# Performance work log

Measured on AMD Instinct MI355X. Metric: run time of the kernel, lower is better.

The kernel has to match this reference:

```python
import jax, jax.numpy as jnp
import numpy as np

D_MODEL, D_K, D_V, H = 64, 32, 32, 8
B, HH, WW = 2, 48, 48
NQ = HH * WW


def setup_inputs() -> dict:
    key = jax.random.key(0)
    ks = jax.random.split(key, 16)
    inp = {
        "queries": jax.random.normal(ks[0], (B, D_MODEL, HH, WW), jnp.float32),
        "keys": jax.random.normal(ks[1], (B, D_MODEL, HH, WW), jnp.float32),
        "values": jax.random.normal(ks[2], (B, D_MODEL, HH, WW), jnp.float32),
        "attention_weights": jax.random.uniform(ks[3], (B, H, NQ, NQ), jnp.float32),
        "attention_mask": jax.random.randint(ks[4], (B, H, NQ, NQ), 0, 2) > 0,
        # Linear params: torch init normal(std=0.001) weights, zero bias
        "Wq": 0.001 * jax.random.normal(ks[5], (H * D_K, D_MODEL), jnp.float32),
        "bq": jnp.zeros((H * D_K,), jnp.float32),
        "Wk": 0.001 * jax.random.normal(ks[6], (H * D_K, D_MODEL), jnp.float32),
        "bk": jnp.zeros((H * D_K,), jnp.float32),
        "Wv": 0.001 * jax.random.normal(ks[7], (H * D_V, D_MODEL), jnp.float32),
        "bv": jnp.zeros((H * D_V,), jnp.float32),
        "Wo": 0.001 * jax.random.normal(ks[8], (D_MODEL, H * D_V), jnp.float32),
        "bo": jnp.zeros((D_MODEL,), jnp.float32),
    }
    return inp


def reference(queries, keys, values, attention_weights, attention_mask,
              Wq, bq, Wk, bk, Wv, bv, Wo, bo):
    b, c, hh, ww = queries.shape
    nq = hh * ww
    # torch .view(b, -1, c) on contiguous (b,c,h,w) is a raw row-major reshape
    qf = queries.reshape(b, nq, c)
    kf = keys.reshape(b, nq, c)
    vf = values.reshape(b, nq, c)
    q = (qf @ Wq.T + bq).reshape(b, nq, H, D_K).transpose(0, 2, 1, 3)  # b h nq dk
    k = (kf @ Wk.T + bk).reshape(b, nq, H, D_K).transpose(0, 2, 1, 3)  # b h nk dk
    v = (vf @ Wv.T + bv).reshape(b, nq, H, D_V).transpose(0, 2, 1, 3)  # b h nk dv
    att = jnp.einsum('bhqd,bhkd->bhqk', q, k) / np.sqrt(D_K).astype(np.float32)
    att = att * attention_weights
    att = jnp.where(attention_mask, -jnp.inf, att)
    att = jax.nn.softmax(att, axis=-1)  # dropout is identity in eval mode
    out = jnp.einsum('bhqk,bhkd->bhqd', att, v)
    out = out.transpose(0, 2, 1, 3).reshape(b, nq, H * D_V)
    out = out @ Wo.T + bo  # (b, nq, d_model)
    return out.reshape(b, -1, hh, ww)  # (b, d_model, h, w)
```

## Files before the change

kernel.cpp:

```cpp
#include <hip/hip_runtime.h>


typedef __attribute__((ext_vector_type(8))) short bf16x8;
typedef __attribute__((ext_vector_type(4))) short bf16x4;
typedef __attribute__((ext_vector_type(4))) float f32x4;
typedef __attribute__((ext_vector_type(4))) unsigned int u32x4;

constexpr int B_  = 2;
constexpr int H_  = 8;
constexpr int NQ_ = 2304;
constexpr int DM_ = 64;
constexpr int DK_ = 32;
constexpr int NT_ = NQ_ / 32;
constexpr int CH_ = 3;
constexpr int TPC_ = NT_ / CH_;
constexpr int GT_ = B_ * H_ * (NQ_ / 16);
constexpr float SCALE_ = 0.17677669529663687f;

constexpr size_t OFF_Q    = 0;
constexpr size_t OFF_K    = 2359296;
constexpr size_t OFF_V    = 4718592;
constexpr size_t OFF_OMID = 7077888;
constexpr size_t OFF_FLAG = 11796480;
constexpr size_t OFF_OP   = 11796736;
constexpr size_t OFF_ML   = 25952512;

static __device__ __forceinline__ unsigned short f2bf(float f) {
    unsigned int u = __builtin_bit_cast(unsigned int, f);
    u += 0x7fffu + ((u >> 16) & 1u);
    return (unsigned short)(u >> 16);
}

__global__ void detect_mask_k(const unsigned int* __restrict__ m, int* __restrict__ flag) {
    int t = threadIdx.x;
    unsigned int v = 0;
    for (int k = 0; k < 16; ++k) v |= m[t * 16 + k];
    unsigned long long b = __ballot(v > 1u);
    if (t == 0) *flag = (b != 0ull) ? 1 : 0;
}

__global__ __launch_bounds__(256) void proj_qkv_k(
    const float* __restrict__ qin, const float* __restrict__ kin, const float* __restrict__ vin,
    const float* __restrict__ Wq, const float* __restrict__ bq,
    const float* __restrict__ Wk, const float* __restrict__ bk,
    const float* __restrict__ Wv, const float* __restrict__ bv,
    unsigned short* __restrict__ Qbf, unsigned short* __restrict__ Kbf,
    unsigned short* __restrict__ Vbf)
{
    const int sel = blockIdx.y;
    const float* in  = sel == 0 ? qin : (sel == 1 ? kin : vin);
    const float* W   = sel == 0 ? Wq  : (sel == 1 ? Wk  : Wv);
    const float* bia = sel == 0 ? bq  : (sel == 1 ? bk  : bv);

    const int rt = blockIdx.x;
    const int b  = rt / (NQ_ / 8);
    const int r0 = (rt % (NQ_ / 8)) * 8;

    __shared__ alignas(16) float ins[8][64];
    const int t = threadIdx.x;
    const float4* src = reinterpret_cast<const float4*>(in + ((size_t)b * NQ_ + r0) * DM_);
    if (t < 128) reinterpret_cast<float4*>(&ins[0][0])[t] = src[t];
    __syncthreads();

    float acc[8];
#pragma unroll
    for (int r = 0; r < 8; ++r) acc[r] = 0.f;
    const float* wrow = W + t * DM_;
    for (int m = 0; m < DM_; ++m) {
        float wv = wrow[m];
#pragma unroll
        for (int r = 0; r < 8; ++r) acc[r] += ins[r][m] * wv;
    }
    const float bb = bia[t];
    const int h = t >> 5, d = t & 31;
#pragma unroll
    for (int r = 0; r < 8; ++r) {
        float o = acc[r] + bb;
        if (sel == 0) o *= SCALE_;
        unsigned short bvv = f2bf(o);
        if (sel == 2) Vbf[(((size_t)b * H_ + h) * DK_ + d) * NQ_ + (r0 + r)] = bvv;
        else {
            unsigned short* out = (sel == 1) ? Kbf : Qbf;
            out[(((size_t)b * H_ + h) * NQ_ + (r0 + r)) * DK_ + d] = bvv;
        }
    }
}

struct KVSlot {
    bf16x8 ka0, ka1;
    bf16x4 v00, v01, v10, v11;
};

static __device__ __forceinline__ void issue_kv(KVSlot& s,
    const unsigned short* __restrict__ kbase, const unsigned short* __restrict__ vbase,
    int j0, int l15, int hi)
{
    s.ka0 = *reinterpret_cast<const bf16x8*>(kbase + (size_t)(j0 + l15) * DK_ + 8 * hi);
    s.ka1 = *reinterpret_cast<const bf16x8*>(kbase + (size_t)(j0 + 16 + l15) * DK_ + 8 * hi);
    s.v00 = *reinterpret_cast<const bf16x4*>(vbase + (size_t)l15 * NQ_ + j0 + 4 * hi);
    s.v01 = *reinterpret_cast<const bf16x4*>(vbase + (size_t)l15 * NQ_ + j0 + 16 + 4 * hi);
    s.v10 = *reinterpret_cast<const bf16x4*>(vbase + (size_t)(16 + l15) * NQ_ + j0 + 4 * hi);
    s.v11 = *reinterpret_cast<const bf16x4*>(vbase + (size_t)(16 + l15) * NQ_ + j0 + 16 + 4 * hi);
}

template<bool ISBYTE> struct MSpan;
template<> struct MSpan<true>  { unsigned int m[8]; };
template<> struct MSpan<false> { u32x4 m[8]; };

static __device__ __forceinline__ void loadW(f32x4 (&W)[8], const float* __restrict__ p) {
#pragma unroll
    for (int u = 0; u < 4; ++u) {
        W[2 * u]     = *reinterpret_cast<const f32x4*>(p + 32 * u);
        W[2 * u + 1] = *reinterpret_cast<const f32x4*>(p + 32 * u + 16);
    }
}

static __device__ __forceinline__ void loadM(MSpan<true>& M, const unsigned char* __restrict__ p) {
#pragma unroll
    for (int u = 0; u < 4; ++u) {
        M.m[2 * u]     = *reinterpret_cast<const unsigned int*>(p + 32 * u);
        M.m[2 * u + 1] = *reinterpret_cast<const unsigned int*>(p + 32 * u + 16);
    }
}
static __device__ __forceinline__ void loadM(MSpan<false>& M, const unsigned char* __restrict__ p) {
#pragma unroll
    for (int u = 0; u < 4; ++u) {
        M.m[2 * u]     = *reinterpret_cast<const u32x4*>(p + 128 * u);
        M.m[2 * u + 1] = *reinterpret_cast<const u32x4*>(p + 128 * u + 64);
    }
}

static __device__ __forceinline__ unsigned int mb32(unsigned int v) { return v; }
static __device__ __forceinline__ unsigned int mb32(u32x4 v) {
    return (v[0] & 1u) | ((v[1] & 1u) << 8) | ((v[2] & 1u) << 16) | ((v[3] & 1u) << 24);
}

template<typename MT>
static __device__ __forceinline__ void consume_tile(
    const KVSlot& s, f32x4 w0, f32x4 w1, MT m0r, MT m1r, bf16x8 qb,
    f32x4& oacc0, f32x4& oacc1, float& lrun)
{
    const f32x4 zero = {0.f, 0.f, 0.f, 0.f};
    f32x4 s0 = __builtin_amdgcn_mfma_f32_16x16x32_bf16(s.ka0, qb, zero, 0, 0, 0);
    f32x4 s1 = __builtin_amdgcn_mfma_f32_16x16x32_bf16(s.ka1, qb, zero, 0, 0, 0);

    const unsigned int ba = mb32(m0r), bb = mb32(m1r);

    float p0[4], p1[4];
#pragma unroll
    for (int r = 0; r < 4; ++r) {
        float e0 = __expf(s0[r] * w0[r]);
        float e1 = __expf(s1[r] * w1[r]);
        p0[r] = ((ba >> (8 * r)) & 0xffu) ? 0.f : e0;
        p1[r] = ((bb >> (8 * r)) & 0xffu) ? 0.f : e1;
    }
    lrun += ((p0[0] + p0[1]) + (p0[2] + p0[3])) + ((p1[0] + p1[1]) + (p1[2] + p1[3]));

    bf16x8 pa;
#pragma unroll
    for (int r = 0; r < 4; ++r) {
        pa[r]     = (short)f2bf(p0[r]);
        pa[4 + r] = (short)f2bf(p1[r]);
    }
    bf16x8 vb0 = __builtin_shufflevector(s.v00, s.v01, 0, 1, 2, 3, 4, 5, 6, 7);
    bf16x8 vb1 = __builtin_shufflevector(s.v10, s.v11, 0, 1, 2, 3, 4, 5, 6, 7);
    oacc0 = __builtin_amdgcn_mfma_f32_16x16x32_bf16(pa, vb0, oacc0, 0, 0, 0);
    oacc1 = __builtin_amdgcn_mfma_f32_16x16x32_bf16(pa, vb1, oacc1, 0, 0, 0);
}

template<bool ISBYTE>
static __device__ __forceinline__ void consume4(
    KVSlot& sA, KVSlot& sB, const f32x4 (&W)[8], const MSpan<ISBYTE>& M,
    int tb, int t1,
    const unsigned short* __restrict__ kbase, const unsigned short* __restrict__ vbase,
    int l15, int hi, bf16x8 qb, f32x4& o0, f32x4& o1, float& lr)
{
    consume_tile(sA, W[0], W[1], M.m[0], M.m[1], qb, o0, o1, lr);
    if (tb + 2 < t1) issue_kv(sA, kbase, vbase, (tb + 2) * 32, l15, hi);
    consume_tile(sB, W[2], W[3], M.m[2], M.m[3], qb, o0, o1, lr);
    if (tb + 3 < t1) issue_kv(sB, kbase, vbase, (tb + 3) * 32, l15, hi);
    consume_tile(sA, W[4], W[5], M.m[4], M.m[5], qb, o0, o1, lr);
    if (tb + 4 < t1) issue_kv(sA, kbase, vbase, (tb + 4) * 32, l15, hi);
    consume_tile(sB, W[6], W[7], M.m[6], M.m[7], qb, o0, o1, lr);
    if (tb + 5 < t1) issue_kv(sB, kbase, vbase, (tb + 5) * 32, l15, hi);
}

template<bool ISBYTE>
static __device__ __forceinline__ void attn_body(
    const unsigned short* __restrict__ Qbf,
    const unsigned short* __restrict__ Kbf,
    const unsigned short* __restrict__ Vbf,
    const float* __restrict__ attw,
    const unsigned char* __restrict__ maskb,
    const int* __restrict__ flagp,
    float* __restrict__ Opart,
    float* __restrict__ MLpart)
{
    if (((*flagp) != 0) != ISBYTE) return;

    const int lane = threadIdx.x & 63;
    const int l15 = lane & 15, hi = lane >> 4;
    const int g = blockIdx.x * 4 + (threadIdx.x >> 6);
    const int chunk = blockIdx.y;
    const int bh = g / (NQ_ / 16);
    const int it = g % (NQ_ / 16);
    const int i0 = it * 16;

    const unsigned short* qbase = Qbf + (size_t)bh * NQ_ * DK_;
    const unsigned short* kbase = Kbf + (size_t)bh * NQ_ * DK_;
    const unsigned short* vbase = Vbf + (size_t)bh * DK_ * NQ_;

    const int q = i0 + l15;
    bf16x8 qb = *reinterpret_cast<const bf16x8*>(qbase + (size_t)q * DK_ + 8 * hi);

    const float* wl = attw + ((size_t)bh * NQ_ + q) * NQ_ + 4 * hi;
    const unsigned char* ml = maskb + (((size_t)bh * NQ_ + q) * NQ_ + 4 * hi) * (ISBYTE ? 1 : 4);

    const int t0 = chunk * TPC_, t1 = t0 + TPC_;
    const size_t msc = ISBYTE ? 1 : 4;

    f32x4 WA[8], WB[8];
    MSpan<ISBYTE> MA, MB;
    KVSlot sA, sB;

    loadW(WA, wl + (size_t)t0 * 32);
    loadM(MA, ml + (size_t)t0 * 32 * msc);
    loadW(WB, wl + (size_t)t0 * 32 + 128);
    loadM(MB, ml + ((size_t)t0 * 32 + 128) * msc);
    issue_kv(sA, kbase, vbase, t0 * 32, l15, hi);
    issue_kv(sB, kbase, vbase, t0 * 32 + 32, l15, hi);

    f32x4 oacc0 = {0.f, 0.f, 0.f, 0.f}, oacc1 = {0.f, 0.f, 0.f, 0.f};
    float lrun = 0.f;

    for (int sp = 0; sp < 3; ++sp) {
        const int tb = t0 + 8 * sp;
        consume4<ISBYTE>(sA, sB, WA, MA, tb, t1, kbase, vbase, l15, hi, qb, oacc0, oacc1, lrun);
        if (sp < 2) {
            loadW(WA, wl + (size_t)(tb + 8) * 32);
            loadM(MA, ml + (size_t)(tb + 8) * 32 * msc);
        }
        consume4<ISBYTE>(sA, sB, WB, MB, tb + 4, t1, kbase, vbase, l15, hi, qb, oacc0, oacc1, lrun);
        if (sp < 2) {
            loadW(WB, wl + (size_t)(tb + 12) * 32);
            loadM(MB, ml + (size_t)(tb + 12) * 32 * msc);
        }
    }

    float* op = Opart + ((size_t)chunk * GT_ + g) * 512;
#pragma unroll
    for (int r = 0; r < 4; ++r) {
        op[(4 * hi + r) * 32 + l15]      = oacc0[r];
        op[(4 * hi + r) * 32 + 16 + l15] = oacc1[r];
    }
    lrun += __shfl_xor(lrun, 16, 64);
    lrun += __shfl_xor(lrun, 32, 64);
    if (hi == 0) {
        float* mlp = MLpart + ((size_t)chunk * GT_ + g) * 32;
        mlp[l15] = lrun;
    }
}

__global__ __launch_bounds__(256, 3) void attn_byte_k(
    const unsigned short* __restrict__ Qbf, const unsigned short* __restrict__ Kbf,
    const unsigned short* __restrict__ Vbf, const float* __restrict__ attw,
    const unsigned char* __restrict__ maskb, const int* __restrict__ flagp,
    float* __restrict__ Opart, float* __restrict__ MLpart)
{
    attn_body<true>(Qbf, Kbf, Vbf, attw, maskb, flagp, Opart, MLpart);
}

__global__ __launch_bounds__(256, 2) void attn_int_k(
    const unsigned short* __restrict__ Qbf, const unsigned short* __restrict__ Kbf,
    const unsigned short* __restrict__ Vbf, const float* __restrict__ attw,
    const unsigned char* __restrict__ maskb, const int* __restrict__ flagp,
    float* __restrict__ Opart, float* __restrict__ MLpart)
{
    attn_body<false>(Qbf, Kbf, Vbf, attw, maskb, flagp, Opart, MLpart);
}

__global__ __launch_bounds__(64) void combine_k(
    const float* __restrict__ Opart, const float* __restrict__ MLpart,
    float* __restrict__ Omid)
{
    const int g = blockIdx.x;
    const int lane = threadIdx.x;
    const int row = lane >> 2;
    const int c4  = (lane & 3) * 8;
    const int bh = g / (NQ_ / 16);
    const int it = g % (NQ_ / 16);
    const int b = bh / H_, h = bh % H_;

    float lg = 0.f;
#pragma unroll
    for (int c = 0; c < CH_; ++c)
        lg += MLpart[((size_t)c * GT_ + g) * 32 + row];
    float inv = 1.0f / lg;

    const size_t ob = (size_t)row * 32 + c4;
    f32x4 a0 = {0.f,0.f,0.f,0.f}, a1 = {0.f,0.f,0.f,0.f};
#pragma unroll
    for (int c = 0; c < CH_; ++c) {
        const float* opp = Opart + ((size_t)c * GT_ + g) * 512 + ob;
        a0 += *reinterpret_cast<const f32x4*>(opp);
        a1 += *reinterpret_cast<const f32x4*>(opp + 4);
    }
    a0 *= inv; a1 *= inv;
    float* dst = Omid + ((size_t)b * NQ_ + it * 16 + row) * 256 + h * 32 + c4;
    *reinterpret_cast<f32x4*>(dst)     = a0;
    *reinterpret_cast<f32x4*>(dst + 4) = a1;
}

__global__ __launch_bounds__(256) void proj_out_k(
    const float* __restrict__ Omid, const float* __restrict__ Wo,
    const float* __restrict__ bo, float* __restrict__ out)
{
    const int rt = blockIdx.x;
    const int b  = rt / (NQ_ / 16);
    const int r0 = (rt % (NQ_ / 16)) * 16;

    __shared__ alignas(16) float lds[16][256];
    const int t = threadIdx.x;
    const float4* src = reinterpret_cast<const float4*>(Omid + ((size_t)b * NQ_ + r0) * 256);
#pragma unroll
    for (int k = 0; k < 4; ++k) reinterpret_cast<float4*>(&lds[0][0])[t + k * 256] = src[t + k * 256];
    __syncthreads();

    const int m = t & 63, rg = t >> 6;
    float acc[4] = {0.f, 0.f, 0.f, 0.f};
    const float* wrow = Wo + m * 256;
    for (int c = 0; c < 256; ++c) {
        float wv = wrow[c];
#pragma unroll
        for (int rr = 0; rr < 4; ++rr) acc[rr] += lds[rg * 4 + rr][c] * wv;
    }
    const float bb = bo[m];
#pragma unroll
    for (int rr = 0; rr < 4; ++rr)
        out[((size_t)b * NQ_ + r0 + rg * 4 + rr) * 64 + m] = acc[rr] + bb;
}

extern "C" void kernel_launch(void* const* d_in, const int* in_sizes, int n_in,
                              void* d_out, int out_size, void* d_ws, size_t ws_size,
                              hipStream_t stream)
{
    (void)in_sizes; (void)n_in; (void)out_size; (void)ws_size;
    const float* qin  = (const float*)d_in[0];
    const float* kin  = (const float*)d_in[1];
    const float* vin  = (const float*)d_in[2];
    const float* attw = (const float*)d_in[3];
    const void*  mask = d_in[4];
    const float* Wq = (const float*)d_in[5];
    const float* bq = (const float*)d_in[6];
    const float* Wk = (const float*)d_in[7];
    const float* bk = (const float*)d_in[8];
    const float* Wv = (const float*)d_in[9];
    const float* bv = (const float*)d_in[10];
    const float* Wo = (const float*)d_in[11];
    const float* bo = (const float*)d_in[12];

    char* ws = (char*)d_ws;
    unsigned short* Qbf   = (unsigned short*)(ws + OFF_Q);
    unsigned short* Kbf   = (unsigned short*)(ws + OFF_K);
    unsigned short* Vbf   = (unsigned short*)(ws + OFF_V);
    float*          Omid  = (float*)(ws + OFF_OMID);
    int*            flag  = (int*)(ws + OFF_FLAG);
    float*          Opart = (float*)(ws + OFF_OP);
    float*          MLp   = (float*)(ws + OFF_ML);

    detect_mask_k<<<1, 64, 0, stream>>>((const unsigned int*)mask, flag);
    proj_qkv_k<<<dim3(B_ * NQ_ / 8, 3), 256, 0, stream>>>(
        qin, kin, vin, Wq, bq, Wk, bk, Wv, bv, Qbf, Kbf, Vbf);
    attn_byte_k<<<dim3(GT_ / 4, CH_), 256, 0, stream>>>(
        Qbf, Kbf, Vbf, attw, (const unsigned char*)mask, flag, Opart, MLp);
    attn_int_k<<<dim3(GT_ / 4, CH_), 256, 0, stream>>>(
        Qbf, Kbf, Vbf, attw, (const unsigned char*)mask, flag, Opart, MLp);
    combine_k<<<GT_, 64, 0, stream>>>(Opart, MLp, Omid);
    proj_out_k<<<B_ * NQ_ / 16, 256, 0, stream>>>(Omid, Wo, bo, (float*)d_out);
}
```

Before: 241.0 us.

## Stage attention weights and mask into an LDS bf16 panel with coalesced loads

Each wavefront now becomes its own 64-thread block. It first loads its 16x768 slice of attention weights and mask with fully coalesced row-wise vector loads, then packs them as bf16 into a swizzled shared-memory panel, encoding masked entries as -1. The main loop reads weights from LDS and uses the sign to apply the mask, and it triple-buffers the K/V loads. This replaces strided per-lane global loads of weights and mask with contiguous streaming, at the cost of 24KB LDS per 64-thread block, which limits occupancy, and an upfront load phase that does not overlap with compute.

```diff
diff --git a/kernel.cpp b/kernel.cpp
--- a/kernel.cpp
+++ b/kernel.cpp
@@ -30,6 +30,9 @@
     u += 0x7fffu + ((u >> 16) & 1u);
     return (unsigned short)(u >> 16);
 }
+static __device__ __forceinline__ float bf2f(short s) {
+    return __builtin_bit_cast(float, ((unsigned int)(unsigned short)s) << 16);
+}
 
 __global__ void detect_mask_k(const unsigned int* __restrict__ m, int* __restrict__ flag) {
     int t = threadIdx.x;
@@ -103,56 +106,23 @@
     s.v11 = *reinterpret_cast<const bf16x4*>(vbase + (size_t)(16 + l15) * NQ_ + j0 + 16 + 4 * hi);
 }
 
-template<bool ISBYTE> struct MSpan;
-template<> struct MSpan<true>  { unsigned int m[8]; };
-template<> struct MSpan<false> { u32x4 m[8]; };
-
-static __device__ __forceinline__ void loadW(f32x4 (&W)[8], const float* __restrict__ p) {
-#pragma unroll
-    for (int u = 0; u < 4; ++u) {
-        W[2 * u]     = *reinterpret_cast<const f32x4*>(p + 32 * u);
-        W[2 * u + 1] = *reinterpret_cast<const f32x4*>(p + 32 * u + 16);
-    }
-}
-
-static __device__ __forceinline__ void loadM(MSpan<true>& M, const unsigned char* __restrict__ p) {
-#pragma unroll
-    for (int u = 0; u < 4; ++u) {
-        M.m[2 * u]     = *reinterpret_cast<const unsigned int*>(p + 32 * u);
-        M.m[2 * u + 1] = *reinterpret_cast<const unsigned int*>(p + 32 * u + 16);
-    }
-}
-static __device__ __forceinline__ void loadM(MSpan<false>& M, const unsigned char* __restrict__ p) {
-#pragma unroll
-    for (int u = 0; u < 4; ++u) {
-        M.m[2 * u]     = *reinterpret_cast<const u32x4*>(p + 128 * u);
-        M.m[2 * u + 1] = *reinterpret_cast<const u32x4*>(p + 128 * u + 64);
-    }
-}
-
-static __device__ __forceinline__ unsigned int mb32(unsigned int v) { return v; }
-static __device__ __forceinline__ unsigned int mb32(u32x4 v) {
-    return (v[0] & 1u) | ((v[1] & 1u) << 8) | ((v[2] & 1u) << 16) | ((v[3] & 1u) << 24);
-}
-
-template<typename MT>
 static __device__ __forceinline__ void consume_tile(
-    const KVSlot& s, f32x4 w0, f32x4 w1, MT m0r, MT m1r, bf16x8 qb,
+    const KVSlot& s, bf16x4 wq0, bf16x4 wq1, bf16x8 qb,
     f32x4& oacc0, f32x4& oacc1, float& lrun)
 {
     const f32x4 zero = {0.f, 0.f, 0.f, 0.f};
     f32x4 s0 = __builtin_amdgcn_mfma_f32_16x16x32_bf16(s.ka0, qb, zero, 0, 0, 0);
     f32x4 s1 = __builtin_amdgcn_mfma_f32_16x16x32_bf16(s.ka1, qb, zero, 0, 0, 0);
 
-    const unsigned int ba = mb32(m0r), bb = mb32(m1r);
-
     float p0[4], p1[4];
 #pragma unroll
     for (int r = 0; r < 4; ++r) {
-        float e0 = __expf(s0[r] * w0[r]);
-        float e1 = __expf(s1[r] * w1[r]);
-        p0[r] = ((ba >> (8 * r)) & 0xffu) ? 0.f : e0;
-        p1[r] = ((bb >> (8 * r)) & 0xffu) ? 0.f : e1;
+        float w0f = bf2f(wq0[r]);
+        float w1f = bf2f(wq1[r]);
+        float e0 = __expf(s0[r] * w0f);
+        float e1 = __expf(s1[r] * w1f);
+        p0[r] = (w0f < 0.f) ? 0.f : e0;
+        p1[r] = (w1f < 0.f) ? 0.f : e1;
     }
     lrun += ((p0[0] + p0[1]) + (p0[2] + p0[3])) + ((p1[0] + p1[1]) + (p1[2] + p1[3]));
 
@@ -166,23 +136,6 @@
     bf16x8 vb1 = __builtin_shufflevector(s.v10, s.v11, 0, 1, 2, 3, 4, 5, 6, 7);
     oacc0 = __builtin_amdgcn_mfma_f32_16x16x32_bf16(pa, vb0, oacc0, 0, 0, 0);
     oacc1 = __builtin_amdgcn_mfma_f32_16x16x32_bf16(pa, vb1, oacc1, 0, 0, 0);
-}
-
-template<bool ISBYTE>
-static __device__ __forceinline__ void consume4(
-    KVSlot& sA, KVSlot& sB, const f32x4 (&W)[8], const MSpan<ISBYTE>& M,
-    int tb, int t1,
-    const unsigned short* __restrict__ kbase, const unsigned short* __restrict__ vbase,
-    int l15, int hi, bf16x8 qb, f32x4& o0, f32x4& o1, float& lr)
-{
-    consume_tile(sA, W[0], W[1], M.m[0], M.m[1], qb, o0, o1, lr);
-    if (tb + 2 < t1) issue_kv(sA, kbase, vbase, (tb + 2) * 32, l15, hi);
-    consume_tile(sB, W[2], W[3], M.m[2], M.m[3], qb, o0, o1, lr);
-    if (tb + 3 < t1) issue_kv(sB, kbase, vbase, (tb + 3) * 32, l15, hi);
-    consume_tile(sA, W[4], W[5], M.m[4], M.m[5], qb, o0, o1, lr);
-    if (tb + 4 < t1) issue_kv(sA, kbase, vbase, (tb + 4) * 32, l15, hi);
-    consume_tile(sB, W[6], W[7], M.m[6], M.m[7], qb, o0, o1, lr);
-    if (tb + 5 < t1) issue_kv(sB, kbase, vbase, (tb + 5) * 32, l15, hi);
 }
 
 template<bool ISBYTE>
@@ -194,13 +147,14 @@
     const unsigned char* __restrict__ maskb,
     const int* __restrict__ flagp,
     float* __restrict__ Opart,
-    float* __restrict__ MLpart)
+    float* __restrict__ MLpart,
+    char* panel)
 {
     if (((*flagp) != 0) != ISBYTE) return;
 
-    const int lane = threadIdx.x & 63;
+    const int lane = threadIdx.x;
     const int l15 = lane & 15, hi = lane >> 4;
-    const int g = blockIdx.x * 4 + (threadIdx.x >> 6);
+    const int g = blockIdx.x;
     const int chunk = blockIdx.y;
     const int bh = g / (NQ_ / 16);
     const int it = g % (NQ_ / 16);
@@ -213,37 +167,92 @@
     const int q = i0 + l15;
     bf16x8 qb = *reinterpret_cast<const bf16x8*>(qbase + (size_t)q * DK_ + 8 * hi);
 
-    const float* wl = attw + ((size_t)bh * NQ_ + q) * NQ_ + 4 * hi;
-    const unsigned char* ml = maskb + (((size_t)bh * NQ_ + q) * NQ_ + 4 * hi) * (ISBYTE ? 1 : 4);
-
-    const int t0 = chunk * TPC_, t1 = t0 + TPC_;
-    const size_t msc = ISBYTE ? 1 : 4;
-
-    f32x4 WA[8], WB[8];
-    MSpan<ISBYTE> MA, MB;
-    KVSlot sA, sB;
-
-    loadW(WA, wl + (size_t)t0 * 32);
-    loadM(MA, ml + (size_t)t0 * 32 * msc);
-    loadW(WB, wl + (size_t)t0 * 32 + 128);
-    loadM(MB, ml + ((size_t)t0 * 32 + 128) * msc);
-    issue_kv(sA, kbase, vbase, t0 * 32, l15, hi);
-    issue_kv(sB, kbase, vbase, t0 * 32 + 32, l15, hi);
-
+    const size_t rowbase = (size_t)(bh * NQ_ + i0) * NQ_ + chunk * 768;
+    const float* wsrc = attw + rowbase;
+
+#pragma unroll
+    for (int bt = 0; bt < 4; ++bt) {
+        f32x4 wv[4][3];
+#pragma unroll
+        for (int rr = 0; rr < 4; ++rr) {
+            const int row = bt * 4 + rr;
+#pragma unroll
+            for (int s = 0; s < 3; ++s)
+                wv[rr][s] = *reinterpret_cast<const f32x4*>(
+                    wsrc + (size_t)row * NQ_ + s * 256 + 4 * lane);
+        }
+        u32x4 mv[4][3];
+        unsigned int mvb[4][3];
+        if constexpr (ISBYTE) {
+            const unsigned char* msrc = maskb + rowbase;
+#pragma unroll
+            for (int rr = 0; rr < 4; ++rr) {
+                const int row = bt * 4 + rr;
+#pragma unroll
+                for (int s = 0; s < 3; ++s)
+                    mvb[rr][s] = *reinterpret_cast<const unsigned int*>(
+                        msrc + (size_t)row * NQ_ + s * 256 + 4 * lane);
+            }
+        } else {
+            const int* msrc = (const int*)maskb + rowbase;
+#pragma unroll
+            for (int rr = 0; rr < 4; ++rr) {
+                const int row = bt * 4 + rr;
+#pragma unroll
+                for (int s = 0; s < 3; ++s)
+                    mv[rr][s] = *reinterpret_cast<const u32x4*>(
+                        msrc + (size_t)row * NQ_ + s * 256 + 4 * lane);
+            }
+        }
+#pragma unroll
+        for (int rr = 0; rr < 4; ++rr) {
+            const int row = bt * 4 + rr;
+#pragma unroll
+            for (int s = 0; s < 3; ++s) {
+                bf16x4 o;
+#pragma unroll
+                for (int k = 0; k < 4; ++k) {
+                    bool msk;
+                    if constexpr (ISBYTE) msk = ((mvb[rr][s] >> (8 * k)) & 0xffu) != 0;
+                    else                  msk = mv[rr][s][k] != 0;
+                    o[k] = msk ? (short)0xBF80 : (short)f2bf(wv[rr][s][k]);
+                }
+                const int off = (row * 1536 + (s * 256 + 4 * lane) * 2) ^ ((row & 7) << 4);
+                *reinterpret_cast<bf16x4*>(panel + off) = o;
+            }
+        }
+    }
+
+    const int jb = chunk * 768;
     f32x4 oacc0 = {0.f, 0.f, 0.f, 0.f}, oacc1 = {0.f, 0.f, 0.f, 0.f};
     float lrun = 0.f;
 
-    for (int sp = 0; sp < 3; ++sp) {
-        const int tb = t0 + 8 * sp;
-        consume4<ISBYTE>(sA, sB, WA, MA, tb, t1, kbase, vbase, l15, hi, qb, oacc0, oacc1, lrun);
-        if (sp < 2) {
-            loadW(WA, wl + (size_t)(tb + 8) * 32);
-            loadM(MA, ml + (size_t)(tb + 8) * 32 * msc);
-        }
-        consume4<ISBYTE>(sA, sB, WB, MB, tb + 4, t1, kbase, vbase, l15, hi, qb, oacc0, oacc1, lrun);
-        if (sp < 2) {
-            loadW(WB, wl + (size_t)(tb + 12) * 32);
-            loadM(MB, ml + (size_t)(tb + 12) * 32 * msc);
+    KVSlot sl0, sl1, sl2;
+    issue_kv(sl0, kbase, vbase, jb, l15, hi);
+    issue_kv(sl1, kbase, vbase, jb + 32, l15, hi);
+    issue_kv(sl2, kbase, vbase, jb + 64, l15, hi);
+
+    const int rb = l15 * 1536;
+    const int sw = (l15 & 7) << 4;
+
+    for (int u = 0; u < TPC_; u += 3) {
+        {
+            bf16x4 wq0 = *reinterpret_cast<const bf16x4*>(panel + ((rb + (u * 32 + 4 * hi) * 2) ^ sw));
+            bf16x4 wq1 = *reinterpret_cast<const bf16x4*>(panel + ((rb + (u * 32 + 16 + 4 * hi) * 2) ^ sw));
+            consume_tile(sl0, wq0, wq1, qb, oacc0, oacc1, lrun);
+            if (u + 3 < TPC_) issue_kv(sl0, kbase, vbase, jb + (u + 3) * 32, l15, hi);
+        }
+        {
+            bf16x4 wq0 = *reinterpret_cast<const bf16x4*>(panel + ((rb + ((u + 1) * 32 + 4 * hi) * 2) ^ sw));
+            bf16x4 wq1 = *reinterpret_cast<const bf16x4*>(panel + ((rb + ((u + 1) * 32 + 16 + 4 * hi) * 2) ^ sw));
+            consume_tile(sl1, wq0, wq1, qb, oacc0, oacc1, lrun);
+            if (u + 4 < TPC_) issue_kv(sl1, kbase, vbase, jb + (u + 4) * 32, l15, hi);
+        }
+        {
+            bf16x4 wq0 = *reinterpret_cast<const bf16x4*>(panel + ((rb + ((u + 2) * 32 + 4 * hi) * 2) ^ sw));
+            bf16x4 wq1 = *reinterpret_cast<const bf16x4*>(panel + ((rb + ((u + 2) * 32 + 16 + 4 * hi) * 2) ^ sw));
+            consume_tile(sl2, wq0, wq1, qb, oacc0, oacc1, lrun);
+            if (u + 5 < TPC_) issue_kv(sl2, kbase, vbase, jb + (u + 5) * 32, l15, hi);
         }
     }
 
@@ -261,22 +270,24 @@
     }
 }
 
-__global__ __launch_bounds__(256, 3) void attn_byte_k(
+__global__ __launch_bounds__(64) void attn_byte_k(
     const unsigned short* __restrict__ Qbf, const unsigned short* __restrict__ Kbf,
     const unsigned short* __restrict__ Vbf, const float* __restrict__ attw,
     const unsigned char* __restrict__ maskb, const int* __restrict__ flagp,
     float* __restrict__ Opart, float* __restrict__ MLpart)
 {
-    attn_body<true>(Qbf, Kbf, Vbf, attw, maskb, flagp, Opart, MLpart);
-}
-
-__global__ __launch_bounds__(256, 2) void attn_int_k(
+    __shared__ alignas(16) char panel[24576];
+    attn_body<true>(Qbf, Kbf, Vbf, attw, maskb, flagp, Opart, MLpart, panel);
+}
+
+__global__ __launch_bounds__(64) void attn_int_k(
     const unsigned short* __restrict__ Qbf, const unsigned short* __restrict__ Kbf,
     const unsigned short* __restrict__ Vbf, const float* __restrict__ attw,
     const unsigned char* __restrict__ maskb, const int* __restrict__ flagp,
     float* __restrict__ Opart, float* __restrict__ MLpart)
 {
-    attn_body<false>(Qbf, Kbf, Vbf, attw, maskb, flagp, Opart, MLpart);
+    __shared__ alignas(16) char panel[24576];
+    attn_body<false>(Qbf, Kbf, Vbf, attw, maskb, flagp, Opart, MLpart, panel);
 }
 
 __global__ __launch_bounds__(64) void combine_k(
@@ -371,9 +382,9 @@
     detect_mask_k<<<1, 64, 0, stream>>>((const unsigned int*)mask, flag);
     proj_qkv_k<<<dim3(B_ * NQ_ / 8, 3), 256, 0, stream>>>(
         qin, kin, vin, Wq, bq, Wk, bk, Wv, bv, Qbf, Kbf, Vbf);
-    attn_byte_k<<<dim3(GT_ / 4, CH_), 256, 0, stream>>>(
+    attn_byte_k<<<dim3(GT_, CH_), 64, 0, stream>>>(
         Qbf, Kbf, Vbf, attw, (const unsigned char*)mask, flag, Opart, MLp);
-    attn_int_k<<<dim3(GT_ / 4, CH_), 256, 0, stream>>>(
+    attn_int_k<<<dim3(GT_, CH_), 64, 0, stream>>>(
         Qbf, Kbf, Vbf, attw, (const unsigned char*)mask, flag, Opart, MLp);
     combine_k<<<GT_, 64, 0, stream>>>(Opart, MLp, Omid);
     proj_out_k<<<B_ * NQ_ / 16, 256, 0, stream>>>(Omid, Wo, bo, (float*)d_out);
```

After: 251.3 us. 1.04x slower.
